# Optimization experiments

Measured on AMD Instinct MI355X. Metric: run time of the kernel, lower is better.

Reference implementation:

```python
import jax, jax.numpy as jnp
import numpy as np

N = 100000      # nodes
E = 2500000     # edges
DIN, H, DOUT = 3, 32, 4
EPS = 1e-5

def _lin(k, i, o):
    kw, kb = jax.random.split(k)
    lim = 1.0 / np.sqrt(i)
    W = jax.random.uniform(kw, (i, o), jnp.float32, -lim, lim)
    b = jax.random.uniform(kb, (o,), jnp.float32, -lim, lim)
    return W, b

def setup_inputs():
    key = jax.random.key(0)
    ks = jax.random.split(key, 12)
    x = jax.random.normal(ks[0], (N, DIN), jnp.float32)
    edge_index = jax.random.randint(ks[1], (2, E), 0, N, dtype=jnp.int32)
    w_in1, b_in1 = _lin(ks[2], DIN, H)
    w_in2, b_in2 = _lin(ks[3], H, H)
    gamma = jnp.ones((H,), jnp.float32)
    beta = jnp.zeros((H,), jnp.float32)
    wg1, bg1 = _lin(ks[4], H, H)
    wg2, bg2 = _lin(ks[5], H, H)
    wg3, bg3 = _lin(ks[6], H, H)
    wo1, bo1 = _lin(ks[7], H, H)
    wo2, bo2 = _lin(ks[8], H, H)
    wo3, bo3 = _lin(ks[9], H, DOUT)
    return dict(x=x, w_in1=w_in1, b_in1=b_in1, w_in2=w_in2, b_in2=b_in2,
                gamma=gamma, beta=beta,
                wg1=wg1, bg1=bg1, wg2=wg2, bg2=bg2, wg3=wg3, bg3=bg3,
                wo1=wo1, bo1=bo1, wo2=wo2, bo2=bo2, wo3=wo3, bo3=bo3,
                edge_index=edge_index)

def _gcn(h, W, b, src, dst, norm):
    # PyG GCNConv: x' = scatter_add(norm * (xW)[src] -> dst) + bias
    hw = h @ W                                   # [N, H]
    msg = hw[src] * norm[:, None]                # [E+N, H] gather + scale
    out = jax.ops.segment_sum(msg, dst, num_segments=N)
    return out + b

def reference(x, w_in1, b_in1, w_in2, b_in2, gamma, beta,
              wg1, bg1, wg2, bg2, wg3, bg3,
              wo1, bo1, wo2, bo2, wo3, bo3, edge_index):
    leaky = lambda v: jax.nn.leaky_relu(v, 0.01)
    # input MLP
    h = leaky(x @ w_in1 + b_in1)
    h = leaky(h @ w_in2 + b_in2)
    # BatchNorm1d (training-mode batch statistics, biased variance)
    mu = jnp.mean(h, axis=0)
    var = jnp.mean((h - mu) ** 2, axis=0)
    h = (h - mu) * jax.lax.rsqrt(var + EPS) * gamma + beta
    # gcn_norm with self-loops: deg over target index, sym normalization
    loop = jnp.arange(N, dtype=edge_index.dtype)
    src = jnp.concatenate([edge_index[0], loop])
    dst = jnp.concatenate([edge_index[1], loop])
    deg = jax.ops.segment_sum(jnp.ones_like(src, jnp.float32), dst, num_segments=N)
    dis = jax.lax.rsqrt(deg)                     # deg >= 1 due to self-loops
    norm = dis[src] * dis[dst]                   # [E+N]
    h = jax.nn.elu(_gcn(h, wg1, bg1, src, dst, norm))
    h = jax.nn.elu(_gcn(h, wg2, bg2, src, dst, norm))
    h = jax.nn.elu(_gcn(h, wg3, bg3, src, dst, norm))
    # output MLP
    r = leaky(h @ wo1 + bo1)
    r = leaky(r @ wo2 + bo2)
    r = r @ wo3 + bo3                            # [N, 4]
    r = r.at[:, 0].set(jax.nn.sigmoid(r[:, 0]))
    return r
```

## Files before the change

kernel.cpp:

```cpp
#include <hip/hip_runtime.h>
#include <hip/hip_fp16.h>

#define HF 32
#define EPS 1e-5f
#define BSH 6
#define BSZ 64
#define CH  16384
#define SUBCAP 320
#define CAP (8*SUBCAP)
#define FXS 524288.0f
#define FXI (1.0f/524288.0f)

typedef int vi4 __attribute__((ext_vector_type(4)));

__device__ __forceinline__ float leaky(float v){ return fmaxf(v, 0.01f*v); }
__device__ __forceinline__ float elu1(float v){ return v > 0.f ? v : (expf(v)-1.f); }
__device__ __forceinline__ float sigmoidf(float v){ return 1.f/(1.f+expf(-v)); }

__device__ __forceinline__ int4 nt_load_i4(const int* p){
    vi4 v = __builtin_nontemporal_load((const vi4*)p);
    return make_int4(v.x, v.y, v.z, v.w);
}

__device__ __forceinline__ void accum8_fx(int* a, float4 v){
    const __half2* p = (const __half2*)&v;
#pragma unroll
    for (int k = 0; k < 4; k++){
        float2 f = __half22float2(p[k]);
        atomicAdd(a + 2*k,     __float2int_rn(f.x * FXS));
        atomicAdd(a + 2*k + 1, __float2int_rn(f.y * FXS));
    }
}

union SMem {
    struct {
        float sW1[3*HF]; float sB1[HF]; float sW2[HF*HF]; float sB2[HF];
        float sh[256][33];
    } mlp;
    struct { int lcnt[2048]; int lbase[2048]; } bin;
};

__global__ __launch_bounds__(256)
void k_mlp_bin(const float* __restrict__ x,
               const float* __restrict__ w1, const float* __restrict__ b1,
               const float* __restrict__ w2, const float* __restrict__ b2,
               __half* __restrict__ h, float* __restrict__ stats,
               const int* __restrict__ src, const int* __restrict__ dst,
               int* __restrict__ gfill, int* __restrict__ ep,
               int N, int E, int B, int NC){
    __shared__ SMem sm;
    int t = threadIdx.x;
    if ((int)blockIdx.x < NC){
        int bid = blockIdx.x;
        for (int i = t; i < B; i += 256) sm.bin.lcnt[i] = 0;
        __syncthreads();
        int base = bid * CH;
        int xcd = bid & 7;
        bool full = (base + CH <= E);
        int rk[64];
        if (full){
#pragma unroll
            for (int i = 0; i < 16; i++){
                int4 d4 = nt_load_i4(dst + base + (t + i*256)*4);
                rk[4*i]   = atomicAdd(&sm.bin.lcnt[d4.x >> BSH], 1);
                rk[4*i+1] = atomicAdd(&sm.bin.lcnt[d4.y >> BSH], 1);
                rk[4*i+2] = atomicAdd(&sm.bin.lcnt[d4.z >> BSH], 1);
                rk[4*i+3] = atomicAdd(&sm.bin.lcnt[d4.w >> BSH], 1);
            }
        } else {
#pragma unroll
            for (int i = 0; i < 64; i++){
                int e = base + t + i*256;
                if (e < E) rk[i] = atomicAdd(&sm.bin.lcnt[dst[e] >> BSH], 1);
            }
        }
        __syncthreads();
        for (int i = t; i < B; i += 256){
            int c = sm.bin.lcnt[i];
            sm.bin.lbase[i] = c ? (i*CAP + xcd*SUBCAP + atomicAdd(&gfill[i*8 + xcd], c)) : 0;
        }
        __syncthreads();
        if (full){
#pragma unroll
            for (int i = 0; i < 16; i++){
                int idx = base + (t + i*256)*4;
                int4 d4 = *(const int4*)(dst + idx);
                int4 s4 = *(const int4*)(src + idx);
                int dd[4] = {d4.x, d4.y, d4.z, d4.w};
                int ss[4] = {s4.x, s4.y, s4.z, s4.w};
#pragma unroll
                for (int k = 0; k < 4; k++){
                    int bb = dd[k] >> BSH;
                    ep[sm.bin.lbase[bb] + rk[4*i+k]] = (ss[k] << BSH) | (dd[k] & (BSZ-1));
                }
            }
        } else {
#pragma unroll
            for (int i = 0; i < 64; i++){
                int e = base + t + i*256;
                if (e < E){
                    int d = dst[e], s = src[e];
                    int bb = d >> BSH;
                    ep[sm.bin.lbase[bb] + rk[i]] = (s << BSH) | (d & (BSZ-1));
                }
            }
        }
    } else {
        for (int i = t; i < 3*HF; i += 256) sm.mlp.sW1[i] = w1[i];
        if (t < HF){ sm.mlp.sB1[t] = b1[t]; sm.mlp.sB2[t] = b2[t]; }
        for (int i = t; i < HF*HF; i += 256) sm.mlp.sW2[i] = w2[i];
        __syncthreads();
        int n = (blockIdx.x - NC)*256 + t;
        float h2[HF];
        if (n < N){
            float x0 = x[(size_t)n*3], x1 = x[(size_t)n*3+1], x2 = x[(size_t)n*3+2];
            float h1[HF];
#pragma unroll
            for (int j = 0; j < HF; j++){
                float v = fmaf(x0, sm.mlp.sW1[j], fmaf(x1, sm.mlp.sW1[HF+j],
                          fmaf(x2, sm.mlp.sW1[2*HF+j], sm.mlp.sB1[j])));
                h1[j] = leaky(v);
            }
#pragma unroll
            for (int j = 0; j < HF; j++){
                float v = sm.mlp.sB2[j];
#pragma unroll
                for (int i = 0; i < HF; i++) v = fmaf(h1[i], sm.mlp.sW2[i*HF+j], v);
                h2[j] = leaky(v);
            }
            float4* hv = (float4*)(h + (size_t)n*HF);
#pragma unroll
            for (int jb = 0; jb < 4; jb++){
                __half2 hh[4];
#pragma unroll
                for (int k = 0; k < 4; k++)
                    hh[k] = __float22half2_rn(make_float2(h2[jb*8+2*k], h2[jb*8+2*k+1]));
                hv[jb] = *(float4*)hh;
            }
        } else {
#pragma unroll
            for (int j = 0; j < HF; j++) h2[j] = 0.f;
        }
#pragma unroll
        for (int j = 0; j < HF; j++) sm.mlp.sh[t][j] = h2[j];
        __syncthreads();
        int f = t & 31, g = t >> 5;
        float s = 0.f, ss = 0.f;
        for (int i = 0; i < 32; i++){
            float v = sm.mlp.sh[g*32 + i][f];
            s += v; ss += v*v;
        }
        __syncthreads();
        sm.mlp.sh[g][f] = s; sm.mlp.sh[8+g][f] = ss;
        __syncthreads();
        if (t < HF){
            float a = 0.f, b = 0.f;
#pragma unroll
            for (int g2 = 0; g2 < 8; g2++){ a += sm.mlp.sh[g2][t]; b += sm.mlp.sh[8+g2][t]; }
            atomicAdd(&stats[t], a);
            atomicAdd(&stats[HF+t], b);
        }
    }
}

__global__ __launch_bounds__(256)
void k_deg_t1(const int* __restrict__ ep, int* __restrict__ ep2,
              const int* __restrict__ gfill,
              int* __restrict__ bcnt, float* __restrict__ dis,
              const __half* __restrict__ h, const float* __restrict__ stats,
              const float* __restrict__ gamma, const float* __restrict__ beta,
              const float* __restrict__ W, __half* __restrict__ tout,
              int N, int B){
    __shared__ union { int sep[CAP]; float hsh[BSZ][HF+1]; } u;
    __shared__ int lcnt[BSZ];
    __shared__ int sbc[64], sbo[64], sbf[64];
    __shared__ float sW[HF*HF];
    __shared__ float sscale[HF], sshift[HF];
    int t = threadIdx.x;
    int b = blockIdx.x;
    for (int i = t; i < HF*HF; i += 256) sW[i] = W[i];
    if (t < HF){
        float inv = 1.0f/(float)N;
        float mu  = stats[t]*inv;
        float var = stats[HF+t]*inv - mu*mu;
        float rs  = rsqrtf(var + EPS);
        float sc  = rs*gamma[t];
        sscale[t] = sc;
        sshift[t] = beta[t] - mu*sc;
    }
    if (t < BSZ) lcnt[t] = 0;
    if (t < 64){ sbc[t] = 0; sbf[t] = 0; }
    int cx[8], coff[8], cnt = 0;
#pragma unroll
    for (int xx = 0; xx < 8; xx++){ cx[xx] = gfill[b*8 + xx]; coff[xx] = cnt; cnt += cx[xx]; }
    int base = b*CAP;
    __syncthreads();
#pragma unroll
    for (int xx = 0; xx < 8; xx++){
        const int* seg = ep + base + xx*SUBCAP;
        for (int j = t; j < cx[xx]; j += 256){
            int v = seg[j];
            u.sep[coff[xx] + j] = v;
            atomicAdd(&lcnt[v & (BSZ-1)], 1);
            atomicAdd(&sbc[v >> 17], 1);
        }
    }
    if (t == 0) bcnt[b] = cnt;
    __syncthreads();
    if (t < 64){
        int val = sbc[t];
#pragma unroll
        for (int off = 1; off < 64; off <<= 1){
            int v2 = __shfl_up(val, off);
            if (t >= off) val += v2;
        }
        sbo[t] = val - sbc[t];
    }
    __syncthreads();
    for (int e = t; e < cnt; e += 256){
        int v = u.sep[e];
        int bin = v >> 17;
        int p = sbo[bin] + atomicAdd(&sbf[bin], 1);
        ep2[base + p] = v;
    }
    __syncthreads();
    int nloc = t >> 2, q = t & 3;
    int n = b*BSZ + nloc;
    float dloc = 0.f;
    if (n < N){
        dloc = rsqrtf((float)lcnt[nloc] + 1.0f);
        if (q == 0) dis[n] = dloc;
        float4 raw = ((const float4*)h)[(size_t)n*4 + q];
        const __half2* p2 = (const __half2*)&raw;
#pragma unroll
        for (int k = 0; k < 4; k++){
            float2 f2 = __half22float2(p2[k]);
            int f = 8*q + 2*k;
            u.hsh[nloc][f]   = fmaf(f2.x, sscale[f],   sshift[f]);
            u.hsh[nloc][f+1] = fmaf(f2.y, sscale[f+1], sshift[f+1]);
        }
    }
    __syncthreads();
    if (n < N){
        int fo = 8*q;
        float o[8] = {0.f,0.f,0.f,0.f,0.f,0.f,0.f,0.f};
#pragma unroll
        for (int i = 0; i < HF; i++){
            float vi = u.hsh[nloc][i];
            float4 w0 = *(const float4*)&sW[i*HF + fo];
            float4 w1 = *(const float4*)&sW[i*HF + fo + 4];
            o[0] = fmaf(vi, w0.x, o[0]); o[1] = fmaf(vi, w0.y, o[1]);
            o[2] = fmaf(vi, w0.z, o[2]); o[3] = fmaf(vi, w0.w, o[3]);
            o[4] = fmaf(vi, w1.x, o[4]); o[5] = fmaf(vi, w1.y, o[5]);
            o[6] = fmaf(vi, w1.z, o[6]); o[7] = fmaf(vi, w1.w, o[7]);
        }
        __half2 hh[4];
#pragma unroll
        for (int k = 0; k < 4; k++)
            hh[k] = __float22half2_rn(make_float2(o[2*k]*dloc, o[2*k+1]*dloc));
        ((float4*)tout)[(size_t)n*4 + q] = *(float4*)hh;
    }
}

__global__ __launch_bounds__(256)
void k_gather_t(const __half* __restrict__ tin, const int* __restrict__ ep,
                const int* __restrict__ bcnt, const float* __restrict__ dis,
                const float* __restrict__ bias, const float* __restrict__ W,
                __half* __restrict__ tout, int N){
    __shared__ int iacc[BSZ][HF+1];
    __shared__ float sW[HF*HF];
    float* facc = (float*)iacc;
    int t = threadIdx.x, b = blockIdx.x;
    for (int i = t; i < HF*HF; i += 256) sW[i] = W[i];
    for (int i = t; i < BSZ*(HF+1); i += 256) ((int*)iacc)[i] = 0;
    int cnt = bcnt[b];
    int base = b*CAP;
    __syncthreads();
    int g = t >> 2, l = t & 3;
    const float4* tv = (const float4*)tin;
    int j = g;
    for (; j + 192 < cnt; j += 256){
        int p0 = ep[base + j];
        int p1 = ep[base + j + 64];
        int p2 = ep[base + j + 128];
        int p3 = ep[base + j + 192];
        float4 r0 = tv[(size_t)(p0 >> BSH)*4 + l];
        float4 r1 = tv[(size_t)(p1 >> BSH)*4 + l];
        float4 r2 = tv[(size_t)(p2 >> BSH)*4 + l];
        float4 r3 = tv[(size_t)(p3 >> BSH)*4 + l];
        accum8_fx(&iacc[p0 & (BSZ-1)][8*l], r0);
        accum8_fx(&iacc[p1 & (BSZ-1)][8*l], r1);
        accum8_fx(&iacc[p2 & (BSZ-1)][8*l], r2);
        accum8_fx(&iacc[p3 & (BSZ-1)][8*l], r3);
    }
    for (; j + 64 < cnt; j += 128){
        int p0 = ep[base + j], p1 = ep[base + j + 64];
        float4 r0 = tv[(size_t)(p0 >> BSH)*4 + l];
        float4 r1 = tv[(size_t)(p1 >> BSH)*4 + l];
        accum8_fx(&iacc[p0 & (BSZ-1)][8*l], r0);
        accum8_fx(&iacc[p1 & (BSZ-1)][8*l], r1);
    }
    for (; j < cnt; j += 64){
        int p0 = ep[base + j];
        float4 r0 = tv[(size_t)(p0 >> BSH)*4 + l];
        accum8_fx(&iacc[p0 & (BSZ-1)][8*l], r0);
    }
    __syncthreads();
    int nloc = t >> 2, q = t & 3;
    int n = b*BSZ + nloc;
    float dv = 0.f;
    float fin[8];
    if (n < N){
        dv = dis[n];
        float4 s0 = tv[(size_t)n*4 + q];
        const __half2* ph = (const __half2*)&s0;
#pragma unroll
        for (int k = 0; k < 4; k++){
            float2 f2 = __half22float2(ph[k]);
            int f = 8*q + 2*k;
            float a0 = (float)iacc[nloc][f]   * FXI + f2.x;
            float a1 = (float)iacc[nloc][f+1] * FXI + f2.y;
            fin[2*k]   = elu1(fmaf(dv, a0, bias[f]));
            fin[2*k+1] = elu1(fmaf(dv, a1, bias[f+1]));
        }
    }
    __syncthreads();
    if (n < N){
#pragma unroll
        for (int k = 0; k < 8; k++) facc[nloc*(HF+1) + 8*q + k] = fin[k];
    }
    __syncthreads();
    if (n < N){
        int fo = 8*q;
        float o[8] = {0.f,0.f,0.f,0.f,0.f,0.f,0.f,0.f};
#pragma unroll
        for (int i = 0; i < HF; i++){
            float hv = facc[nloc*(HF+1) + i];
            float4 w0 = *(const float4*)&sW[i*HF + fo];
            float4 w1 = *(const float4*)&sW[i*HF + fo + 4];
            o[0] = fmaf(hv, w0.x, o[0]); o[1] = fmaf(hv, w0.y, o[1]);
            o[2] = fmaf(hv, w0.z, o[2]); o[3] = fmaf(hv, w0.w, o[3]);
            o[4] = fmaf(hv, w1.x, o[4]); o[5] = fmaf(hv, w1.y, o[5]);
            o[6] = fmaf(hv, w1.z, o[6]); o[7] = fmaf(hv, w1.w, o[7]);
        }
        __half2 hh[4];
#pragma unroll
        for (int k = 0; k < 4; k++)
            hh[k] = __float22half2_rn(make_float2(o[2*k]*dv, o[2*k+1]*dv));
        ((float4*)tout)[(size_t)n*4 + q] = *(float4*)hh;
    }
}

__global__ __launch_bounds__(256)
void k_gather_out(const __half* __restrict__ tin, const int* __restrict__ ep,
                  const int* __restrict__ bcnt, const float* __restrict__ dis,
                  const float* __restrict__ bg3,
                  const float* __restrict__ wo1, const float* __restrict__ bo1,
                  const float* __restrict__ wo2, const float* __restrict__ bo2,
                  const float* __restrict__ wo3, const float* __restrict__ bo3,
                  float* __restrict__ out, int N){
    __shared__ int iacc[BSZ][HF+1];
    __shared__ float sW1[HF*HF], sW2[HF*HF], sW3[HF*4];
    float* facc = (float*)iacc;
    int t = threadIdx.x, b = blockIdx.x;
    for (int i = t; i < HF*HF; i += 256){ sW1[i] = wo1[i]; sW2[i] = wo2[i]; }
    if (t < HF*4) sW3[t] = wo3[t];
    for (int i = t; i < BSZ*(HF+1); i += 256) ((int*)iacc)[i] = 0;
    int cnt = bcnt[b];
    int base = b*CAP;
    __syncthreads();
    int g = t >> 2, l = t & 3;
    const float4* tv = (const float4*)tin;
    int j = g;
    for (; j + 192 < cnt; j += 256){
        int p0 = ep[base + j];
        int p1 = ep[base + j + 64];
        int p2 = ep[base + j + 128];
        int p3 = ep[base + j + 192];
        float4 r0 = tv[(size_t)(p0 >> BSH)*4 + l];
        float4 r1 = tv[(size_t)(p1 >> BSH)*4 + l];
        float4 r2 = tv[(size_t)(p2 >> BSH)*4 + l];
        float4 r3 = tv[(size_t)(p3 >> BSH)*4 + l];
        accum8_fx(&iacc[p0 & (BSZ-1)][8*l], r0);
        accum8_fx(&iacc[p1 & (BSZ-1)][8*l], r1);
        accum8_fx(&iacc[p2 & (BSZ-1)][8*l], r2);
        accum8_fx(&iacc[p3 & (BSZ-1)][8*l], r3);
    }
    for (; j + 64 < cnt; j += 128){
        int p0 = ep[base + j], p1 = ep[base + j + 64];
        float4 r0 = tv[(size_t)(p0 >> BSH)*4 + l];
        float4 r1 = tv[(size_t)(p1 >> BSH)*4 + l];
        accum8_fx(&iacc[p0 & (BSZ-1)][8*l], r0);
        accum8_fx(&iacc[p1 & (BSZ-1)][8*l], r1);
    }
    for (; j < cnt; j += 64){
        int p0 = ep[base + j];
        float4 r0 = tv[(size_t)(p0 >> BSH)*4 + l];
        accum8_fx(&iacc[p0 & (BSZ-1)][8*l], r0);
    }
    __syncthreads();
    int nloc = t >> 2, q = t & 3;
    int n = b*BSZ + nloc;
    float fin[8];
    if (n < N){
        float dv = dis[n];
        float4 s0 = tv[(size_t)n*4 + q];
        const __half2* ph = (const __half2*)&s0;
#pragma unroll
        for (int k = 0; k < 4; k++){
            float2 f2 = __half22float2(ph[k]);
            int f = 8*q + 2*k;
            float a0 = (float)iacc[nloc][f]   * FXI + f2.x;
            float a1 = (float)iacc[nloc][f+1] * FXI + f2.y;
            fin[2*k]   = elu1(fmaf(dv, a0, bg3[f]));
            fin[2*k+1] = elu1(fmaf(dv, a1, bg3[f+1]));
        }
    }
    __syncthreads();
    if (n < N){
#pragma unroll
        for (int k = 0; k < 8; k++) facc[nloc*(HF+1) + 8*q + k] = fin[k];
    }
    __syncthreads();
    float o1[8];
    if (n < N){
        int fo = 8*q;
#pragma unroll
        for (int c = 0; c < 8; c++) o1[c] = bo1[fo + c];
#pragma unroll
        for (int i = 0; i < HF; i++){
            float hv = facc[nloc*(HF+1) + i];
            float4 w0 = *(const float4*)&sW1[i*HF + fo];
            float4 w1 = *(const float4*)&sW1[i*HF + fo + 4];
            o1[0] = fmaf(hv, w0.x, o1[0]); o1[1] = fmaf(hv, w0.y, o1[1]);
            o1[2] = fmaf(hv, w0.z, o1[2]); o1[3] = fmaf(hv, w0.w, o1[3]);
            o1[4] = fmaf(hv, w1.x, o1[4]); o1[5] = fmaf(hv, w1.y, o1[5]);
            o1[6] = fmaf(hv, w1.z, o1[6]); o1[7] = fmaf(hv, w1.w, o1[7]);
        }
    }
    __syncthreads();
    if (n < N){
        int fo = 8*q;
#pragma unroll
        for (int c = 0; c < 8; c++) facc[nloc*(HF+1) + fo + c] = leaky(o1[c]);
    }
    __syncthreads();
    float o2[8];
    if (n < N){
        int fo = 8*q;
#pragma unroll
        for (int c = 0; c < 8; c++) o2[c] = bo2[fo + c];
#pragma unroll
        for (int i = 0; i < HF; i++){
            float hv = facc[nloc*(HF+1) + i];
            float4 w0 = *(const float4*)&sW2[i*HF + fo];
            float4 w1 = *(const float4*)&sW2[i*HF + fo + 4];
            o2[0] = fmaf(hv, w0.x, o2[0]); o2[1] = fmaf(hv, w0.y, o2[1]);
            o2[2] = fmaf(hv, w0.z, o2[2]); o2[3] = fmaf(hv, w0.w, o2[3]);
            o2[4] = fmaf(hv, w1.x, o2[4]); o2[5] = fmaf(hv, w1.y, o2[5]);
            o2[6] = fmaf(hv, w1.z, o2[6]); o2[7] = fmaf(hv, w1.w, o2[7]);
        }
    }
    __syncthreads();
    if (n < N){
        int fo = 8*q;
#pragma unroll
        for (int c = 0; c < 8; c++) facc[nloc*(HF+1) + fo + c] = leaky(o2[c]);
    }
    __syncthreads();
    if (n < N){
        float v = bo3[q];
#pragma unroll
        for (int i = 0; i < HF; i++) v = fmaf(facc[nloc*(HF+1) + i], sW3[i*4 + q], v);
        if (q == 0) v = sigmoidf(v);
        out[(size_t)n*4 + q] = v;
    }
}

extern "C" void kernel_launch(void* const* d_in, const int* in_sizes, int n_in,
                              void* d_out, int out_size, void* d_ws, size_t ws_size,
                              hipStream_t stream) {
    const float* x     = (const float*)d_in[0];
    const float* w_in1 = (const float*)d_in[1];
    const float* b_in1 = (const float*)d_in[2];
    const float* w_in2 = (const float*)d_in[3];
    const float* b_in2 = (const float*)d_in[4];
    const float* gamma = (const float*)d_in[5];
    const float* beta  = (const float*)d_in[6];
    const float* wg1   = (const float*)d_in[7];
    const float* bg1   = (const float*)d_in[8];
    const float* wg2   = (const float*)d_in[9];
    const float* bg2   = (const float*)d_in[10];
    const float* wg3   = (const float*)d_in[11];
    const float* bg3   = (const float*)d_in[12];
    const float* wo1   = (const float*)d_in[13];
    const float* bo1   = (const float*)d_in[14];
    const float* wo2   = (const float*)d_in[15];
    const float* bo2   = (const float*)d_in[16];
    const float* wo3   = (const float*)d_in[17];
    const float* bo3   = (const float*)d_in[18];
    const int*   ei    = (const int*)d_in[19];

    int N = in_sizes[0] / 3;
    int E = in_sizes[19] / 2;
    int B = (N + BSZ - 1) >> BSH;

    char* w = (char*)d_ws;
    size_t o = 0;
    auto alloc = [&](size_t bytes){ size_t r = o; o = (o + bytes + 255) & ~(size_t)255; return r; };
    float* stats = (float*)(w + alloc(2*HF*sizeof(float)));
    int*   gfill = (int*)  (w + alloc((size_t)B*8*4));
    size_t zero_bytes = o;
    int*   bcnt  = (int*)  (w + alloc((size_t)B*4));
    float* dis   = (float*)(w + alloc((size_t)N*4));
    int*   ep    = (int*)  (w + alloc((size_t)B*CAP*4));
    int*   ep2   = (int*)  (w + alloc((size_t)B*CAP*4));
    __half* bufH = (__half*)(w + alloc((size_t)N*HF*2));
    __half* tA   = (__half*)(w + alloc((size_t)N*HF*2));
    __half* tB   = (__half*)(w + alloc((size_t)N*HF*2));

    hipMemsetAsync(d_ws, 0, zero_bytes, stream);

    const int* src = ei;
    const int* dst = ei + E;
    int NB1 = (N + 255) / 256;
    int NC  = (E + CH - 1) / CH;

    k_mlp_bin<<<NC + NB1, 256, 0, stream>>>(x, w_in1, b_in1, w_in2, b_in2, bufH, stats,
                                            src, dst, gfill, ep, N, E, B, NC);
    k_deg_t1<<<B, 256, 0, stream>>>(ep, ep2, gfill, bcnt, dis,
                                    bufH, stats, gamma, beta, wg1, tA, N, B);
    k_gather_t<<<B, 256, 0, stream>>>(tA, ep2, bcnt, dis, bg1, wg2, tB, N);
    k_gather_t<<<B, 256, 0, stream>>>(tB, ep2, bcnt, dis, bg2, wg3, tA, N);
    k_gather_out<<<B, 256, 0, stream>>>(tA, ep2, bcnt, dis, bg3,
                                        wo1, bo1, wo2, bo2, wo3, bo3, (float*)d_out, N);
}
```

Baseline: 257.5 us.

## Merge edge binning and input MLP into one uniform block grid

Instead of launching separate binning blocks and MLP blocks, every block now bins a chunk of edges sized from E/NB1 (rounded to 256) and then runs the input MLP and BatchNorm stats for its 256 nodes. The goal is to balance work across blocks and remove the tail where a few heavy binning blocks, each handling 16384 edges, finish after the MLP blocks. The trade-off is that the vectorized nontemporal int4 loads are replaced by scalar strided loads. There are also more per-block global atomics on gfill, and each block now runs the two phases back to back. Coverage is only complete when E fits within NB1*EPT*256.

```diff
diff --git a/kernel.cpp b/kernel.cpp
--- a/kernel.cpp
+++ b/kernel.cpp
@@ -5,11 +5,11 @@
 #define EPS 1e-5f
 #define BSH 6
 #define BSZ 64
-#define CH  16384
 #define SUBCAP 320
 #define CAP (8*SUBCAP)
 #define FXS 524288.0f
 #define FXI (1.0f/524288.0f)
+#define EPT 32
 
 typedef int vi4 __attribute__((ext_vector_type(4)));
 
@@ -47,32 +47,21 @@
                __half* __restrict__ h, float* __restrict__ stats,
                const int* __restrict__ src, const int* __restrict__ dst,
                int* __restrict__ gfill, int* __restrict__ ep,
-               int N, int E, int B, int NC){
+               int N, int E, int B, int CH2){
     __shared__ SMem sm;
     int t = threadIdx.x;
-    if ((int)blockIdx.x < NC){
-        int bid = blockIdx.x;
+    int bid = blockIdx.x;
+    {
         for (int i = t; i < B; i += 256) sm.bin.lcnt[i] = 0;
         __syncthreads();
-        int base = bid * CH;
+        int base = bid * CH2;
         int xcd = bid & 7;
-        bool full = (base + CH <= E);
-        int rk[64];
-        if (full){
-#pragma unroll
-            for (int i = 0; i < 16; i++){
-                int4 d4 = nt_load_i4(dst + base + (t + i*256)*4);
-                rk[4*i]   = atomicAdd(&sm.bin.lcnt[d4.x >> BSH], 1);
-                rk[4*i+1] = atomicAdd(&sm.bin.lcnt[d4.y >> BSH], 1);
-                rk[4*i+2] = atomicAdd(&sm.bin.lcnt[d4.z >> BSH], 1);
-                rk[4*i+3] = atomicAdd(&sm.bin.lcnt[d4.w >> BSH], 1);
-            }
-        } else {
-#pragma unroll
-            for (int i = 0; i < 64; i++){
-                int e = base + t + i*256;
-                if (e < E) rk[i] = atomicAdd(&sm.bin.lcnt[dst[e] >> BSH], 1);
-            }
+        int rk[EPT];
+#pragma unroll
+        for (int i = 0; i < EPT; i++){
+            int e = base + t + i*256;
+            if (i*256 < CH2 && e < E)
+                rk[i] = atomicAdd(&sm.bin.lcnt[dst[e] >> BSH], 1);
         }
         __syncthreads();
         for (int i = t; i < B; i += 256){
@@ -80,86 +69,70 @@
             sm.bin.lbase[i] = c ? (i*CAP + xcd*SUBCAP + atomicAdd(&gfill[i*8 + xcd], c)) : 0;
         }
         __syncthreads();
-        if (full){
-#pragma unroll
-            for (int i = 0; i < 16; i++){
-                int idx = base + (t + i*256)*4;
-                int4 d4 = *(const int4*)(dst + idx);
-                int4 s4 = *(const int4*)(src + idx);
-                int dd[4] = {d4.x, d4.y, d4.z, d4.w};
-                int ss[4] = {s4.x, s4.y, s4.z, s4.w};
-#pragma unroll
-                for (int k = 0; k < 4; k++){
-                    int bb = dd[k] >> BSH;
-                    ep[sm.bin.lbase[bb] + rk[4*i+k]] = (ss[k] << BSH) | (dd[k] & (BSZ-1));
-                }
+#pragma unroll
+        for (int i = 0; i < EPT; i++){
+            int e = base + t + i*256;
+            if (i*256 < CH2 && e < E){
+                int d = dst[e], s = src[e];
+                int bb = d >> BSH;
+                ep[sm.bin.lbase[bb] + rk[i]] = (s << BSH) | (d & (BSZ-1));
             }
-        } else {
-#pragma unroll
-            for (int i = 0; i < 64; i++){
-                int e = base + t + i*256;
-                if (e < E){
-                    int d = dst[e], s = src[e];
-                    int bb = d >> BSH;
-                    ep[sm.bin.lbase[bb] + rk[i]] = (s << BSH) | (d & (BSZ-1));
-                }
-            }
+        }
+    }
+    __syncthreads();
+    for (int i = t; i < 3*HF; i += 256) sm.mlp.sW1[i] = w1[i];
+    if (t < HF){ sm.mlp.sB1[t] = b1[t]; sm.mlp.sB2[t] = b2[t]; }
+    for (int i = t; i < HF*HF; i += 256) sm.mlp.sW2[i] = w2[i];
+    __syncthreads();
+    int n = bid*256 + t;
+    float h2[HF];
+    if (n < N){
+        float x0 = x[(size_t)n*3], x1 = x[(size_t)n*3+1], x2 = x[(size_t)n*3+2];
+        float h1[HF];
+#pragma unroll
+        for (int j = 0; j < HF; j++){
+            float v = fmaf(x0, sm.mlp.sW1[j], fmaf(x1, sm.mlp.sW1[HF+j],
+                      fmaf(x2, sm.mlp.sW1[2*HF+j], sm.mlp.sB1[j])));
+            h1[j] = leaky(v);
+        }
+#pragma unroll
+        for (int j = 0; j < HF; j++){
+            float v = sm.mlp.sB2[j];
+#pragma unroll
+            for (int i = 0; i < HF; i++) v = fmaf(h1[i], sm.mlp.sW2[i*HF+j], v);
+            h2[j] = leaky(v);
+        }
+        float4* hv = (float4*)(h + (size_t)n*HF);
+#pragma unroll
+        for (int jb = 0; jb < 4; jb++){
+            __half2 hh[4];
+#pragma unroll
+            for (int k = 0; k < 4; k++)
+                hh[k] = __float22half2_rn(make_float2(h2[jb*8+2*k], h2[jb*8+2*k+1]));
+            hv[jb] = *(float4*)hh;
         }
     } else {
-        for (int i = t; i < 3*HF; i += 256) sm.mlp.sW1[i] = w1[i];
-        if (t < HF){ sm.mlp.sB1[t] = b1[t]; sm.mlp.sB2[t] = b2[t]; }
-        for (int i = t; i < HF*HF; i += 256) sm.mlp.sW2[i] = w2[i];
-        __syncthreads();
-        int n = (blockIdx.x - NC)*256 + t;
-        float h2[HF];
-        if (n < N){
-            float x0 = x[(size_t)n*3], x1 = x[(size_t)n*3+1], x2 = x[(size_t)n*3+2];
-            float h1[HF];
-#pragma unroll
-            for (int j = 0; j < HF; j++){
-                float v = fmaf(x0, sm.mlp.sW1[j], fmaf(x1, sm.mlp.sW1[HF+j],
-                          fmaf(x2, sm.mlp.sW1[2*HF+j], sm.mlp.sB1[j])));
-                h1[j] = leaky(v);
-            }
-#pragma unroll
-            for (int j = 0; j < HF; j++){
-                float v = sm.mlp.sB2[j];
-#pragma unroll
-                for (int i = 0; i < HF; i++) v = fmaf(h1[i], sm.mlp.sW2[i*HF+j], v);
-                h2[j] = leaky(v);
-            }
-            float4* hv = (float4*)(h + (size_t)n*HF);
-#pragma unroll
-            for (int jb = 0; jb < 4; jb++){
-                __half2 hh[4];
-#pragma unroll
-                for (int k = 0; k < 4; k++)
-                    hh[k] = __float22half2_rn(make_float2(h2[jb*8+2*k], h2[jb*8+2*k+1]));
-                hv[jb] = *(float4*)hh;
-            }
-        } else {
-#pragma unroll
-            for (int j = 0; j < HF; j++) h2[j] = 0.f;
-        }
-#pragma unroll
-        for (int j = 0; j < HF; j++) sm.mlp.sh[t][j] = h2[j];
-        __syncthreads();
-        int f = t & 31, g = t >> 5;
-        float s = 0.f, ss = 0.f;
-        for (int i = 0; i < 32; i++){
-            float v = sm.mlp.sh[g*32 + i][f];
-            s += v; ss += v*v;
-        }
-        __syncthreads();
-        sm.mlp.sh[g][f] = s; sm.mlp.sh[8+g][f] = ss;
-        __syncthreads();
-        if (t < HF){
-            float a = 0.f, b = 0.f;
-#pragma unroll
-            for (int g2 = 0; g2 < 8; g2++){ a += sm.mlp.sh[g2][t]; b += sm.mlp.sh[8+g2][t]; }
-            atomicAdd(&stats[t], a);
-            atomicAdd(&stats[HF+t], b);
-        }
+#pragma unroll
+        for (int j = 0; j < HF; j++) h2[j] = 0.f;
+    }
+#pragma unroll
+    for (int j = 0; j < HF; j++) sm.mlp.sh[t][j] = h2[j];
+    __syncthreads();
+    int f = t & 31, g = t >> 5;
+    float s = 0.f, ss = 0.f;
+    for (int i = 0; i < 32; i++){
+        float v = sm.mlp.sh[g*32 + i][f];
+        s += v; ss += v*v;
+    }
+    __syncthreads();
+    sm.mlp.sh[g][f] = s; sm.mlp.sh[8+g][f] = ss;
+    __syncthreads();
+    if (t < HF){
+        float a = 0.f, b2 = 0.f;
+#pragma unroll
+        for (int g2 = 0; g2 < 8; g2++){ a += sm.mlp.sh[g2][t]; b2 += sm.mlp.sh[8+g2][t]; }
+        atomicAdd(&stats[t], a);
+        atomicAdd(&stats[HF+t], b2);
     }
 }
 
@@ -524,10 +497,11 @@
     const int* src = ei;
     const int* dst = ei + E;
     int NB1 = (N + 255) / 256;
-    int NC  = (E + CH - 1) / CH;
-
-    k_mlp_bin<<<NC + NB1, 256, 0, stream>>>(x, w_in1, b_in1, w_in2, b_in2, bufH, stats,
-                                            src, dst, gfill, ep, N, E, B, NC);
+    int CH2 = ((E + NB1 - 1) / NB1 + 255) & ~255;
+    if (CH2 > EPT*256) CH2 = EPT*256;
+
+    k_mlp_bin<<<NB1, 256, 0, stream>>>(x, w_in1, b_in1, w_in2, b_in2, bufH, stats,
+                                       src, dst, gfill, ep, N, E, B, CH2);
     k_deg_t1<<<B, 256, 0, stream>>>(ep, ep2, gfill, bcnt, dis,
                                     bufH, stats, gamma, beta, wg1, tA, N, B);
     k_gather_t<<<B, 256, 0, stream>>>(tA, ep2, bcnt, dis, bg1, wg2, tB, N);
```

Result: no change. 260.1 us (+1.0%).

## Replace global atomic bucket fill with per-chunk local prefix-sum offsets

Applied to the files above, without the earlier changes.

Binning no longer reserves slots through global atomics into per-XCD sub-buckets. Each chunk now does a block-local exclusive scan over bucket counts, writes its edges contiguously inside its own chunk region, and records per-bucket offsets in an NC×(B+1) table. The degree kernel then has one thread per chunk read that chunk's segment for the bucket and place it using a block scan. This removes global atomic contention and fixed sub-bucket capacity, but each gathering thread copies its segment serially, and the scan assumes NC ≤ 256 and B ≤ 2048.

```diff
diff --git a/kernel.cpp b/kernel.cpp
--- a/kernel.cpp
+++ b/kernel.cpp
@@ -6,8 +6,7 @@
 #define BSH 6
 #define BSZ 64
 #define CH  16384
-#define SUBCAP 320
-#define CAP (8*SUBCAP)
+#define CAP 2560
 #define FXS 524288.0f
 #define FXI (1.0f/524288.0f)
 
@@ -37,7 +36,7 @@
         float sW1[3*HF]; float sB1[HF]; float sW2[HF*HF]; float sB2[HF];
         float sh[256][33];
     } mlp;
-    struct { int lcnt[2048]; int lbase[2048]; } bin;
+    struct { int lcnt[2048]; int lbase[2048]; int wsum[4]; } bin;
 };
 
 __global__ __launch_bounds__(256)
@@ -46,17 +45,17 @@
                const float* __restrict__ w2, const float* __restrict__ b2,
                __half* __restrict__ h, float* __restrict__ stats,
                const int* __restrict__ src, const int* __restrict__ dst,
-               int* __restrict__ gfill, int* __restrict__ ep,
+               int* __restrict__ offs, int* __restrict__ ep,
                int N, int E, int B, int NC){
     __shared__ SMem sm;
     int t = threadIdx.x;
     if ((int)blockIdx.x < NC){
         int bid = blockIdx.x;
-        for (int i = t; i < B; i += 256) sm.bin.lcnt[i] = 0;
+        for (int i = t; i < 2048; i += 256) sm.bin.lcnt[i] = 0;
         __syncthreads();
         int base = bid * CH;
-        int xcd = bid & 7;
         bool full = (base + CH <= E);
+        int cntblk = full ? CH : (E - base);
         int rk[64];
         if (full){
 #pragma unroll
@@ -75,11 +74,30 @@
             }
         }
         __syncthreads();
-        for (int i = t; i < B; i += 256){
-            int c = sm.bin.lcnt[i];
-            sm.bin.lbase[i] = c ? (i*CAP + xcd*SUBCAP + atomicAdd(&gfill[i*8 + xcd], c)) : 0;
-        }
-        __syncthreads();
+        {
+            int vals[8], ssum = 0;
+            int t8 = t*8;
+#pragma unroll
+            for (int k = 0; k < 8; k++){ vals[k] = sm.bin.lcnt[t8+k]; ssum += vals[k]; }
+            int lane = t & 63, wv = t >> 6;
+            int v = ssum;
+#pragma unroll
+            for (int off = 1; off < 64; off <<= 1){
+                int u2 = __shfl_up(v, off);
+                if (lane >= off) v += u2;
+            }
+            if (lane == 63) sm.bin.wsum[wv] = v;
+            __syncthreads();
+            int woff = 0;
+            for (int j2 = 0; j2 < wv; j2++) woff += sm.bin.wsum[j2];
+            int run = woff + v - ssum;
+#pragma unroll
+            for (int k = 0; k < 8; k++){ sm.bin.lbase[t8+k] = run; run += vals[k]; }
+        }
+        __syncthreads();
+        int* orow = offs + (size_t)bid*(B+1);
+        for (int i = t; i < B; i += 256) orow[i] = sm.bin.lbase[i];
+        if (t == 0) orow[B] = cntblk;
         if (full){
 #pragma unroll
             for (int i = 0; i < 16; i++){
@@ -91,7 +109,7 @@
 #pragma unroll
                 for (int k = 0; k < 4; k++){
                     int bb = dd[k] >> BSH;
-                    ep[sm.bin.lbase[bb] + rk[4*i+k]] = (ss[k] << BSH) | (dd[k] & (BSZ-1));
+                    ep[base + sm.bin.lbase[bb] + rk[4*i+k]] = (ss[k] << BSH) | (dd[k] & (BSZ-1));
                 }
             }
         } else {
@@ -101,7 +119,7 @@
                 if (e < E){
                     int d = dst[e], s = src[e];
                     int bb = d >> BSH;
-                    ep[sm.bin.lbase[bb] + rk[i]] = (s << BSH) | (d & (BSZ-1));
+                    ep[base + sm.bin.lbase[bb] + rk[i]] = (s << BSH) | (d & (BSZ-1));
                 }
             }
         }
@@ -165,15 +183,16 @@
 
 __global__ __launch_bounds__(256)
 void k_deg_t1(const int* __restrict__ ep, int* __restrict__ ep2,
-              const int* __restrict__ gfill,
+              const int* __restrict__ offs,
               int* __restrict__ bcnt, float* __restrict__ dis,
               const __half* __restrict__ h, const float* __restrict__ stats,
               const float* __restrict__ gamma, const float* __restrict__ beta,
               const float* __restrict__ W, __half* __restrict__ tout,
-              int N, int B){
+              int N, int B, int NC){
     __shared__ union { int sep[CAP]; float hsh[BSZ][HF+1]; } u;
     __shared__ int lcnt[BSZ];
     __shared__ int sbc[64], sbo[64], sbf[64];
+    __shared__ int wsum4[4];
     __shared__ float sW[HF*HF];
     __shared__ float sscale[HF], sshift[HF];
     int t = threadIdx.x;
@@ -190,22 +209,35 @@
     }
     if (t < BSZ) lcnt[t] = 0;
     if (t < 64){ sbc[t] = 0; sbf[t] = 0; }
-    int cx[8], coff[8], cnt = 0;
-#pragma unroll
-    for (int xx = 0; xx < 8; xx++){ cx[xx] = gfill[b*8 + xx]; coff[xx] = cnt; cnt += cx[xx]; }
-    int base = b*CAP;
-    __syncthreads();
-#pragma unroll
-    for (int xx = 0; xx < 8; xx++){
-        const int* seg = ep + base + xx*SUBCAP;
-        for (int j = t; j < cx[xx]; j += 256){
-            int v = seg[j];
-            u.sep[coff[xx] + j] = v;
-            atomicAdd(&lcnt[v & (BSZ-1)], 1);
-            atomicAdd(&sbc[v >> 17], 1);
-        }
-    }
+    int myst = 0, mylen = 0;
+    if (t < NC){
+        const int* op = offs + (size_t)t*(B+1) + b;
+        myst  = op[0];
+        mylen = op[1] - op[0];
+    }
+    int lane = t & 63, wv = t >> 6;
+    int v = mylen;
+#pragma unroll
+    for (int off = 1; off < 64; off <<= 1){
+        int u2 = __shfl_up(v, off);
+        if (lane >= off) v += u2;
+    }
+    if (lane == 63) wsum4[wv] = v;
+    __syncthreads();
+    int woff = 0;
+    for (int j2 = 0; j2 < wv; j2++) woff += wsum4[j2];
+    int dst0 = woff + v - mylen;
+    int cnt = wsum4[0] + wsum4[1] + wsum4[2] + wsum4[3];
     if (t == 0) bcnt[b] = cnt;
+    if (t < NC && mylen > 0){
+        const int* sp = ep + (size_t)t*CH + myst;
+        for (int k = 0; k < mylen; k++){
+            int vv = sp[k];
+            u.sep[dst0 + k] = vv;
+            atomicAdd(&lcnt[vv & (BSZ-1)], 1);
+            atomicAdd(&sbc[vv >> 17], 1);
+        }
+    }
     __syncthreads();
     if (t < 64){
         int val = sbc[t];
@@ -218,10 +250,10 @@
     }
     __syncthreads();
     for (int e = t; e < cnt; e += 256){
-        int v = u.sep[e];
-        int bin = v >> 17;
+        int vv = u.sep[e];
+        int bin = vv >> 17;
         int p = sbo[bin] + atomicAdd(&sbf[bin], 1);
-        ep2[base + p] = v;
+        ep2[(size_t)b*CAP + p] = vv;
     }
     __syncthreads();
     int nloc = t >> 2, q = t & 3;
@@ -274,7 +306,7 @@
     for (int i = t; i < HF*HF; i += 256) sW[i] = W[i];
     for (int i = t; i < BSZ*(HF+1); i += 256) ((int*)iacc)[i] = 0;
     int cnt = bcnt[b];
-    int base = b*CAP;
+    size_t base = (size_t)b*CAP;
     __syncthreads();
     int g = t >> 2, l = t & 3;
     const float4* tv = (const float4*)tin;
@@ -367,7 +399,7 @@
     if (t < HF*4) sW3[t] = wo3[t];
     for (int i = t; i < BSZ*(HF+1); i += 256) ((int*)iacc)[i] = 0;
     int cnt = bcnt[b];
-    int base = b*CAP;
+    size_t base = (size_t)b*CAP;
     __syncthreads();
     int g = t >> 2, l = t & 3;
     const float4* tv = (const float4*)tin;
@@ -504,16 +536,17 @@
     int N = in_sizes[0] / 3;
     int E = in_sizes[19] / 2;
     int B = (N + BSZ - 1) >> BSH;
+    int NC = (E + CH - 1) / CH;
 
     char* w = (char*)d_ws;
     size_t o = 0;
     auto alloc = [&](size_t bytes){ size_t r = o; o = (o + bytes + 255) & ~(size_t)255; return r; };
     float* stats = (float*)(w + alloc(2*HF*sizeof(float)));
-    int*   gfill = (int*)  (w + alloc((size_t)B*8*4));
     size_t zero_bytes = o;
+    int*   offs  = (int*)  (w + alloc((size_t)NC*(B+1)*4));
     int*   bcnt  = (int*)  (w + alloc((size_t)B*4));
     float* dis   = (float*)(w + alloc((size_t)N*4));
-    int*   ep    = (int*)  (w + alloc((size_t)B*CAP*4));
+    int*   ep    = (int*)  (w + alloc((size_t)NC*CH*4));
     int*   ep2   = (int*)  (w + alloc((size_t)B*CAP*4));
     __half* bufH = (__half*)(w + alloc((size_t)N*HF*2));
     __half* tA   = (__half*)(w + alloc((size_t)N*HF*2));
@@ -524,12 +557,11 @@
     const int* src = ei;
     const int* dst = ei + E;
     int NB1 = (N + 255) / 256;
-    int NC  = (E + CH - 1) / CH;
 
     k_mlp_bin<<<NC + NB1, 256, 0, stream>>>(x, w_in1, b_in1, w_in2, b_in2, bufH, stats,
-                                            src, dst, gfill, ep, N, E, B, NC);
-    k_deg_t1<<<B, 256, 0, stream>>>(ep, ep2, gfill, bcnt, dis,
-                                    bufH, stats, gamma, beta, wg1, tA, N, B);
+                                            src, dst, offs, ep, N, E, B, NC);
+    k_deg_t1<<<B, 256, 0, stream>>>(ep, ep2, offs, bcnt, dis,
+                                    bufH, stats, gamma, beta, wg1, tA, N, B, NC);
     k_gather_t<<<B, 256, 0, stream>>>(tA, ep2, bcnt, dis, bg1, wg2, tB, N);
     k_gather_t<<<B, 256, 0, stream>>>(tB, ep2, bcnt, dis, bg2, wg3, tA, N);
     k_gather_out<<<B, 256, 0, stream>>>(tA, ep2, bcnt, dis, bg3,
```

Result: slower. 263.1 us (+2.1%).
